# Optimization experiments

Hardware: AMD Instinct MI355X
Metric: run time of the kernel (lower is better)

The kernel has to match this reference:

```python
import jax, jax.numpy as jnp
import numpy as np

B, A, E = 16384, 8, 512


def setup_inputs() -> dict:
    key = jax.random.key(0)
    ks = jax.random.split(key, 6)
    return {
        "image_features": jax.random.normal(ks[0], (B, E), dtype=jnp.float32),
        "edge_attributes": jax.random.normal(ks[1], (B, A, E), dtype=jnp.float32),
        "linear_w": jax.random.normal(ks[2], (E, 2 * E), dtype=jnp.float32) * (1.0 / np.sqrt(2 * E)),
        "linear_b": jax.random.normal(ks[3], (E,), dtype=jnp.float32) * 0.01,
        "fwd_proj": jax.random.normal(ks[4], (A, E, E), dtype=jnp.float32) * (1.0 / np.sqrt(E)),
        "bwd_proj": jax.random.normal(ks[5], (A, E, E), dtype=jnp.float32) * (1.0 / np.sqrt(E)),
        "self_weighted": jnp.ones((1, A, 1), dtype=jnp.float32),
    }


def reference(image_features, edge_attributes, linear_w, linear_b, fwd_proj, bwd_proj, self_weighted):
    # Forward attribute GNN: broadcast src over attribute axis, concat, linear(2E->E)
    src = jnp.broadcast_to(image_features[:, None, :], edge_attributes.shape)  # [B,A,E]
    x = jnp.concatenate([src, edge_attributes], axis=-1)                       # [B,A,2E]
    agg = jnp.einsum('bak,ek->bae', x, linear_w) + linear_b                    # [B,A,E]
    attr_rep = jnp.einsum('bai,aij->baj', agg, fwd_proj)                       # [B,A,E]

    # Backward attribute GNN: per-type projection, ReLU, learned weighted sum over A
    proj = jnp.einsum('bai,aij->baj', attr_rep, bwd_proj)                      # [B,A,E]
    individuals = jnp.sum(jax.nn.relu(proj) * self_weighted, axis=1)           # [B,E]
    return attr_rep, individuals
```

## Files before the change

### kernel.cpp

```cpp
#include <hip/hip_runtime.h>
#include <cstdint>
#include <cstddef>

#define NB 16384
#define NA 8
#define NE 512
#define NK 1024
#define NN 4096

typedef __bf16 bf16x8 __attribute__((ext_vector_type(8)));
typedef float  f32x4  __attribute__((ext_vector_type(4)));
typedef uint16_t u16x8 __attribute__((ext_vector_type(8)));

__device__ __forceinline__ uint16_t cvt_bf16(float f) {
    uint32_t u = __builtin_bit_cast(uint32_t, f);
    u += 0x7fffu + ((u >> 16) & 1u);
    return (uint16_t)(u >> 16);
}

__device__ __forceinline__ int swz(int row) { return (row ^ (row >> 2)) & 3; }

__device__ __forceinline__ int cf_pos(int row, int c) {
    return ((row >> 1) << 3) + ((((row & 1) << 2) + c) ^ ((row >> 1) & 7));
}

__device__ __forceinline__ void gl_lds16(const void* g, void* l) {
    __builtin_amdgcn_global_load_lds(
        (__attribute__((address_space(1))) void*)(void*)g,
        (__attribute__((address_space(3))) void*)l, 16, 0, 0);
}

__device__ __forceinline__ void tcvt_tile(const float* __restrict__ src,
                                          uint16_t* __restrict__ dst,
                                          int R, int C, int c0, int r0, int t) {
    __shared__ float tile[32][33];
    int tx = t & 31, ty = t >> 5;
#pragma unroll
    for (int yy = 0; yy < 4; ++yy) {
        int r = ty + yy * 8;
        tile[r][tx] = src[(size_t)(r0 + r) * C + c0 + tx];
    }
    __syncthreads();
#pragma unroll
    for (int yy = 0; yy < 4; ++yy) {
        int c = ty + yy * 8;
        dst[(size_t)(c0 + c) * R + r0 + tx] = cvt_bf16(tile[tx][c]);
    }
}

__global__ __launch_bounds__(256) void k_pre(const float* __restrict__ lw,
                                             const float* __restrict__ fwd,
                                             const float* __restrict__ bwd,
                                             const float* __restrict__ img,
                                             const float* __restrict__ lb,
                                             uint16_t* __restrict__ lwT,
                                             uint16_t* __restrict__ fwdT,
                                             uint16_t* __restrict__ bwdT,
                                             uint16_t* __restrict__ imgb,
                                             float* __restrict__ bvec) {
    int b = blockIdx.x, t = threadIdx.x;
    if (b < 512) {
        int bx = b & 31, by = b >> 5;
        tcvt_tile(lw, lwT, NE, NK, bx * 32, by * 32, t);
    } else if (b < 2560) {
        int i = b - 512;
        int mat = i >> 8, bx = i & 15, by = (i >> 4) & 15;
        tcvt_tile(fwd + (size_t)mat * NE * NE, fwdT + (size_t)mat * NE * NE,
                  NE, NE, bx * 32, by * 32, t);
    } else if (b < 4608) {
        int i = b - 2560;
        int mat = i >> 8, bx = i & 15, by = (i >> 4) & 15;
        tcvt_tile(bwd + (size_t)mat * NE * NE, bwdT + (size_t)mat * NE * NE,
                  NE, NE, bx * 32, by * 32, t);
    } else if (b < 12800) {
        int i = (b - 4608) * 256 + t;
        float4 v = ((const float4*)img)[i];
        ushort4 o;
        o.x = cvt_bf16(v.x); o.y = cvt_bf16(v.y); o.z = cvt_bf16(v.z); o.w = cvt_bf16(v.w);
        ((ushort4*)imgb)[i] = o;
    } else {
        int i = b - 12800;
        int a = i >> 4, i0 = (i & 15) * 32;
        float s0 = 0.f, s1 = 0.f;
#pragma unroll 4
        for (int k = 0; k < 32; ++k) {
            float w = lb[i0 + k];
            const float* f = fwd + ((size_t)a * NE + i0 + k) * NE;
            s0 = fmaf(w, f[t], s0);
            s1 = fmaf(w, f[t + 256], s1);
        }
        atomicAdd(&bvec[a * NE + t], s0);
        atomicAdd(&bvec[a * NE + t + 256], s1);
    }
}

__global__ __launch_bounds__(256) void k_prep(const uint16_t* __restrict__ lwT,
                                              const uint16_t* __restrict__ fwdT,
                                              uint16_t* __restrict__ TMT) {
    __shared__ alignas(16) uint16_t lA[128 * 32];
    __shared__ alignas(16) uint16_t lB[128 * 32];
    int bz = blockIdx.x;
    int nt = bz & 31, mt = bz >> 5;
    int m0 = mt * 128, n0 = nt * 128;
    int t = threadIdx.x, lane = t & 63;
    int w = t >> 6, wm = w >> 1, wn = w & 1;
    int lr = lane & 15, lc = lane >> 4;
    int sl = swz(lr);
    f32x4 acc[4][4] = {};
    for (int k0 = 0; k0 < NE; k0 += 32) {
        __syncthreads();
#pragma unroll
        for (int p = 0; p < 2; ++p) {
            int idx = p * 256 + t;
            int row = idx >> 2, c16 = (idx & 3) ^ swz(row);
            gl_lds16(lwT + (size_t)(m0 + row) * NE + k0 + c16 * 8, lA + idx * 8);
            gl_lds16(fwdT + (size_t)(n0 + row) * NE + k0 + c16 * 8, lB + idx * 8);
        }
        __syncthreads();
        bf16x8 af[4], bfr[4];
#pragma unroll
        for (int i = 0; i < 4; ++i)
            af[i] = *(const bf16x8*)&lA[(wm * 64 + i * 16 + lr) * 32 + ((lc ^ sl) << 3)];
#pragma unroll
        for (int j = 0; j < 4; ++j)
            bfr[j] = *(const bf16x8*)&lB[(wn * 64 + j * 16 + lr) * 32 + ((lc ^ sl) << 3)];
#pragma unroll
        for (int i = 0; i < 4; ++i)
#pragma unroll
            for (int j = 0; j < 4; ++j)
                acc[i][j] = __builtin_amdgcn_mfma_f32_16x16x32_bf16(af[i], bfr[j], acc[i][j], 0, 0, 0);
    }
#pragma unroll
    for (int i = 0; i < 4; ++i) {
        int mb = m0 + wm * 64 + i * 16 + lc * 4;
#pragma unroll
        for (int j = 0; j < 4; ++j) {
            int n = n0 + wn * 64 + j * 16 + lr;
            ushort4 v;
            v.x = cvt_bf16(acc[i][j][0]);
            v.y = cvt_bf16(acc[i][j][1]);
            v.z = cvt_bf16(acc[i][j][2]);
            v.w = cvt_bf16(acc[i][j][3]);
            *(ushort4*)&TMT[(size_t)n * NK + mb] = v;
        }
    }
}

template<bool WB>
__global__ __launch_bounds__(512) void k_mm4(const uint16_t* __restrict__ imgb,
                                             const float* __restrict__ edge,
                                             const uint16_t* __restrict__ TMT,
                                             const float* __restrict__ bvec,
                                             float* __restrict__ attr,
                                             uint16_t* __restrict__ attrb) {
    __shared__ alignas(16) uint16_t lA[2][128 * 32];
    __shared__ alignas(16) uint16_t lB[2][256 * 32];
    int o = blockIdx.x;
    int a = o & 7, idx = o >> 3;
    int jt = idx & 1, mt = idx >> 1;
    int m0 = mt * 128, jb = jt * 256;
    int t = threadIdx.x, lane = t & 63;
    int w = t >> 6, wm = w >> 2, wn = w & 3;
    int lr = lane & 15, lc = lane >> 4;
    int rpA = t >> 3, qA = (t & 7) ^ (rpA & 7);
    int srA = (rpA << 1) | (qA >> 2), scA = (qA & 3) << 3;
    int srB[2], scB[2];
#pragma unroll
    for (int p = 0; p < 2; ++p) {
        int u = t + p * 512;
        int rp = u >> 3, q = (u & 7) ^ (rp & 7);
        srB[p] = (rp << 1) | (q >> 2);
        scB[p] = (q & 3) << 3;
    }
    int er = t >> 2, ec = t & 3;
    int epos = cf_pos(er, ec) * 8;
    int aoff[4], boff[4];
#pragma unroll
    for (int i = 0; i < 4; ++i) {
        aoff[i] = cf_pos(wm * 64 + i * 16 + lr, lc) * 8;
        boff[i] = cf_pos(wn * 64 + i * 16 + lr, lc) * 8;
    }
    auto stage_img = [&](int buf, int s) {
        gl_lds16(imgb + (size_t)(m0 + srA) * NE + s * 32 + scA, &lA[buf][t * 8]);
    };
    auto stage_tmt = [&](int buf, int s) {
#pragma unroll
        for (int p = 0; p < 2; ++p)
            gl_lds16(TMT + (size_t)(a * NE + jb + srB[p]) * NK + s * 32 + scB[p],
                     &lB[buf][(t + p * 512) * 8]);
    };
    f32x4 acc[4][4] = {};
    stage_img(0, 0);
    stage_tmt(0, 0);
    for (int s = 0; s < 32; ++s) {
        int cur = s & 1, nb = cur ^ 1;
        __syncthreads();
        float4 e0, e1;
        bool eN = (s < 31) && (s + 1 >= 16);
        if (s < 31) {
            if (s + 1 < 16) {
                stage_img(nb, s + 1);
            } else {
                int kk = (s + 1 - 16) * 32;
                const float* sp = edge + ((size_t)(m0 + er) * NA + a) * NE + kk + ec * 8;
                e0 = ((const float4*)sp)[0];
                e1 = ((const float4*)sp)[1];
            }
            stage_tmt(nb, s + 1);
        }
        bf16x8 af[4], bfr[4];
#pragma unroll
        for (int i = 0; i < 4; ++i) af[i] = *(const bf16x8*)&lA[cur][aoff[i]];
#pragma unroll
        for (int j = 0; j < 4; ++j) bfr[j] = *(const bf16x8*)&lB[cur][boff[j]];
#pragma unroll
        for (int i = 0; i < 4; ++i)
#pragma unroll
            for (int j = 0; j < 4; ++j)
                acc[i][j] = __builtin_amdgcn_mfma_f32_16x16x32_bf16(af[i], bfr[j], acc[i][j], 0, 0, 0);
        if (eN) {
            u16x8 ov = {cvt_bf16(e0.x), cvt_bf16(e0.y), cvt_bf16(e0.z), cvt_bf16(e0.w),
                        cvt_bf16(e1.x), cvt_bf16(e1.y), cvt_bf16(e1.z), cvt_bf16(e1.w)};
            *(u16x8*)&lA[nb][epos] = ov;
        }
    }
#pragma unroll
    for (int j = 0; j < 4; ++j) {
        float bv = bvec[a * NE + jb + wn * 64 + j * 16 + lr];
#pragma unroll
        for (int i = 0; i < 4; ++i)
#pragma unroll
            for (int r = 0; r < 4; ++r)
                acc[i][j][r] += bv;
    }
#pragma unroll
    for (int i = 0; i < 4; ++i) {
#pragma unroll
        for (int r = 0; r < 4; ++r) {
            int bm = m0 + wm * 64 + i * 16 + lc * 4 + r;
            float* orow = attr + ((size_t)bm * NA + a) * NE + jb;
#pragma unroll
            for (int j = 0; j < 4; ++j)
                __builtin_nontemporal_store(acc[i][j][r], &orow[wn * 64 + j * 16 + lr]);
            if (WB) {
                uint16_t* brw = attrb + ((size_t)bm * NA + a) * NE + jb;
#pragma unroll
                for (int j = 0; j < 4; ++j)
                    brw[wn * 64 + j * 16 + lr] = cvt_bf16(acc[i][j][r]);
            }
        }
    }
}

template<bool AB>
__global__ __launch_bounds__(256) void k_ind4(const float* __restrict__ attrf,
                                              const uint16_t* __restrict__ attrb,
                                              const uint16_t* __restrict__ bwdT,
                                              const float* __restrict__ sw,
                                              float* __restrict__ ind) {
    __shared__ alignas(16) uint16_t lA[2][128 * 32];
    __shared__ alignas(16) uint16_t lB[2][128 * 32];
    int o = blockIdx.x;
    int xcd = o & 7, mt = o >> 3;
    int jt = xcd >> 1, ah = xcd & 1;
    int m0 = mt * 128, jb = jt * 128, a0 = ah * 4;
    int t = threadIdx.x, lane = t & 63;
    int w = t >> 6, wm = w >> 1, wn = w & 1;
    int lr = lane & 15, lc = lane >> 4;
    int srow[2], sc8[2];
#pragma unroll
    for (int p = 0; p < 2; ++p) {
        int u = p * 256 + t;
        int rp = u >> 3, q = (u & 7) ^ (rp & 7);
        srow[p] = (rp << 1) | (q >> 2);
        sc8[p] = (q & 3) << 3;
    }
    int erow[2], ec[2], epos[2];
#pragma unroll
    for (int p = 0; p < 2; ++p) {
        int u = p * 256 + t;
        erow[p] = u >> 2; ec[p] = u & 3;
        epos[p] = cf_pos(erow[p], ec[p]) * 8;
    }
    int aoff[4], boff[4];
#pragma unroll
    for (int i = 0; i < 4; ++i) {
        aoff[i] = cf_pos(wm * 64 + i * 16 + lr, lc) * 8;
        boff[i] = cf_pos(wn * 64 + i * 16 + lr, lc) * 8;
    }
    auto stage = [&](int buf, int s) {
        int aa = a0 + (s >> 4), kk = (s & 15) * 32;
        if (AB) {
#pragma unroll
            for (int p = 0; p < 2; ++p)
                gl_lds16(attrb + ((size_t)(m0 + srow[p]) * NA + aa) * NE + kk + sc8[p],
                         &lA[buf][(p * 256 + t) * 8]);
        } else {
#pragma unroll
            for (int p = 0; p < 2; ++p) {
                const float* sp = attrf + ((size_t)(m0 + erow[p]) * NA + aa) * NE + kk + ec[p] * 8;
                float4 v0 = ((const float4*)sp)[0];
                float4 v1 = ((const float4*)sp)[1];
                u16x8 ov = {cvt_bf16(v0.x), cvt_bf16(v0.y), cvt_bf16(v0.z), cvt_bf16(v0.w),
                            cvt_bf16(v1.x), cvt_bf16(v1.y), cvt_bf16(v1.z), cvt_bf16(v1.w)};
                *(u16x8*)&lA[buf][epos[p]] = ov;
            }
        }
#pragma unroll
        for (int p = 0; p < 2; ++p)
            gl_lds16(bwdT + (size_t)(aa * NE + jb + srow[p]) * NE + kk + sc8[p],
                     &lB[buf][(p * 256 + t) * 8]);
    };
    f32x4 res[4][4] = {};
    f32x4 acc[4][4] = {};
    stage(0, 0);
    for (int s = 0; s < 64; ++s) {
        int cur = s & 1;
        __syncthreads();
        if (s < 63) stage(cur ^ 1, s + 1);
        bf16x8 af[4], bfr[4];
#pragma unroll
        for (int i = 0; i < 4; ++i) af[i] = *(const bf16x8*)&lA[cur][aoff[i]];
#pragma unroll
        for (int j = 0; j < 4; ++j) bfr[j] = *(const bf16x8*)&lB[cur][boff[j]];
#pragma unroll
        for (int i = 0; i < 4; ++i)
#pragma unroll
            for (int j = 0; j < 4; ++j)
                acc[i][j] = __builtin_amdgcn_mfma_f32_16x16x32_bf16(af[i], bfr[j], acc[i][j], 0, 0, 0);
        if ((s & 15) == 15) {
            float wa = sw[a0 + (s >> 4)];
#pragma unroll
            for (int i = 0; i < 4; ++i)
#pragma unroll
                for (int j = 0; j < 4; ++j) {
#pragma unroll
                    for (int r = 0; r < 4; ++r)
                        res[i][j][r] += wa * fmaxf(acc[i][j][r], 0.f);
                    acc[i][j] = (f32x4){0.f, 0.f, 0.f, 0.f};
                }
        }
    }
#pragma unroll
    for (int i = 0; i < 4; ++i) {
#pragma unroll
        for (int r = 0; r < 4; ++r) {
            int bm = m0 + wm * 64 + i * 16 + lc * 4 + r;
            float* orow = ind + (size_t)bm * NE + jb;
#pragma unroll
            for (int j = 0; j < 4; ++j)
                atomicAdd(&orow[wn * 64 + j * 16 + lr], res[i][j][r]);
        }
    }
}

extern "C" void kernel_launch(void* const* d_in, const int* in_sizes, int n_in,
                              void* d_out, int out_size, void* d_ws, size_t ws_size,
                              hipStream_t stream) {
    (void)in_sizes; (void)n_in; (void)out_size;
    const float* img  = (const float*)d_in[0];
    const float* edge = (const float*)d_in[1];
    const float* lw   = (const float*)d_in[2];
    const float* lb   = (const float*)d_in[3];
    const float* fwd  = (const float*)d_in[4];
    const float* bwd  = (const float*)d_in[5];
    const float* sw   = (const float*)d_in[6];
    float* attr = (float*)d_out;
    float* ind  = attr + (size_t)NB * NA * NE;

    char* ws = (char*)d_ws;
    size_t off = 0;
    auto alloc = [&](size_t bytes) { void* p = ws + off; off += bytes; return p; };
    uint16_t* lwT  = (uint16_t*)alloc((size_t)NK * NE * 2);
    uint16_t* fwdT = (uint16_t*)alloc((size_t)NA * NE * NE * 2);
    uint16_t* bwdT = (uint16_t*)alloc((size_t)NA * NE * NE * 2);
    uint16_t* TMT  = (uint16_t*)alloc((size_t)NN * NK * 2);
    uint16_t* imgb = (uint16_t*)alloc((size_t)NB * NE * 2);
    float*    bvec = (float*)alloc((size_t)NN * 4);

    const size_t BIGB = (size_t)NB * NA * NE * 2;
    bool has_attrb = ws_size >= off + BIGB;
    uint16_t* attrb = has_attrb ? (uint16_t*)alloc(BIGB) : (uint16_t*)0;

    hipMemsetAsync(bvec, 0, (size_t)NN * 4, stream);
    hipMemsetAsync(ind, 0, (size_t)NB * NE * 4, stream);

    k_pre<<<12928, 256, 0, stream>>>(lw, fwd, bwd, img, lb, lwT, fwdT, bwdT, imgb, bvec);
    k_prep<<<(NK / 128) * (NN / 128), 256, 0, stream>>>(lwT, fwdT, TMT);

    int mm_grid = 8 * 2 * (NB / 128);
    int ind_grid = (NB / 128) * (NE / 128) * 2;

    if (has_attrb) {
        k_mm4<true><<<mm_grid, 512, 0, stream>>>(imgb, edge, TMT, bvec, attr, attrb);
        k_ind4<true><<<ind_grid, 256, 0, stream>>>(attr, attrb, bwdT, sw, ind);
    } else {
        k_mm4<false><<<mm_grid, 512, 0, stream>>>(imgb, edge, TMT, bvec, attr, attrb);
        k_ind4<false><<<ind_grid, 256, 0, stream>>>(attr, attrb, bwdT, sw, ind);
    }
}
```

Before: 440.6 us.

## Pre-convert edge attributes to bf16 and use triple-buffered async-LDS GEMM

Adds a pre-pass in k_pre that converts the large edge_attributes tensor to bf16 in workspace. A new k_mm10 kernel then streams both A and B operands with direct global-to-LDS loads in 64-wide K chunks, triple-buffered with swizzled LDS. The aim is to drop the fp32 register-staged conversion from the main GEMM and overlap loads with MFMA. The cost is an extra full pass over edge (read fp32, write bf16) and extra workspace, and the path only runs when the workspace is large enough.

```diff
diff --git a/kernel.cpp b/kernel.cpp
--- a/kernel.cpp
+++ b/kernel.cpp
@@ -53,11 +53,13 @@
                                              const float* __restrict__ bwd,
                                              const float* __restrict__ img,
                                              const float* __restrict__ lb,
+                                             const float* __restrict__ edge,
                                              uint16_t* __restrict__ lwT,
                                              uint16_t* __restrict__ fwdT,
                                              uint16_t* __restrict__ bwdT,
                                              uint16_t* __restrict__ imgb,
-                                             float* __restrict__ bvec) {
+                                             float* __restrict__ bvec,
+                                             uint16_t* __restrict__ edgeb) {
     int b = blockIdx.x, t = threadIdx.x;
     if (b < 512) {
         int bx = b & 31, by = b >> 5;
@@ -78,7 +80,7 @@
         ushort4 o;
         o.x = cvt_bf16(v.x); o.y = cvt_bf16(v.y); o.z = cvt_bf16(v.z); o.w = cvt_bf16(v.w);
         ((ushort4*)imgb)[i] = o;
-    } else {
+    } else if (b < 12928) {
         int i = b - 12800;
         int a = i >> 4, i0 = (i & 15) * 32;
         float s0 = 0.f, s1 = 0.f;
@@ -91,6 +93,14 @@
         }
         atomicAdd(&bvec[a * NE + t], s0);
         atomicAdd(&bvec[a * NE + t + 256], s1);
+    } else {
+        size_t i8 = (size_t)(b - 12928) * 256 + t;
+        const float* sp = edge + i8 * 8;
+        float4 v0 = ((const float4*)sp)[0];
+        float4 v1 = ((const float4*)sp)[1];
+        u16x8 o = {cvt_bf16(v0.x), cvt_bf16(v0.y), cvt_bf16(v0.z), cvt_bf16(v0.w),
+                   cvt_bf16(v1.x), cvt_bf16(v1.y), cvt_bf16(v1.z), cvt_bf16(v1.w)};
+        *(u16x8*)(edgeb + i8 * 8) = o;
     }
 }
 
@@ -142,6 +152,128 @@
             v.z = cvt_bf16(acc[i][j][2]);
             v.w = cvt_bf16(acc[i][j][3]);
             *(ushort4*)&TMT[(size_t)n * NK + mb] = v;
+        }
+    }
+}
+
+template<bool WB>
+__global__ __launch_bounds__(512) void k_mm10(const uint16_t* __restrict__ imgb,
+                                              const uint16_t* __restrict__ edgeb,
+                                              const uint16_t* __restrict__ TMT,
+                                              const float* __restrict__ bvec,
+                                              float* __restrict__ attr,
+                                              uint16_t* __restrict__ attrb) {
+    __shared__ alignas(16) uint16_t lA[3][128 * 64];
+    __shared__ alignas(16) uint16_t lB[3][256 * 64];
+    int o = blockIdx.x;
+    int a = o & 7, idx = o >> 3;
+    int jt = idx & 1, mt = idx >> 1;
+    int m0 = mt * 128, jb = jt * 256;
+    int t = threadIdx.x, lane = t & 63;
+    int w = t >> 6, wm = w >> 2, wn = w & 3;
+    int lr = lane & 15, lc = lane >> 4;
+    int srA[2], scA[2];
+#pragma unroll
+    for (int p = 0; p < 2; ++p) {
+        int u = t + p * 512;
+        srA[p] = u >> 3;
+        scA[p] = ((u & 7) ^ (srA[p] & 7)) << 3;
+    }
+    int srB[4], scB[4];
+#pragma unroll
+    for (int p = 0; p < 4; ++p) {
+        int u = t + p * 512;
+        srB[p] = u >> 3;
+        scB[p] = ((u & 7) ^ (srB[p] & 7)) << 3;
+    }
+    int arow[4], brow[4];
+#pragma unroll
+    for (int i = 0; i < 4; ++i) {
+        arow[i] = wm * 64 + i * 16 + lr;
+        brow[i] = wn * 64 + i * 16 + lr;
+    }
+    f32x4 acc[4][4] = {};
+
+    auto stage = [&](int buf, int k) {
+        if (k < 8) {
+#pragma unroll
+            for (int p = 0; p < 2; ++p)
+                gl_lds16(imgb + (size_t)(m0 + srA[p]) * NE + k * 64 + scA[p],
+                         &lA[buf][(t + p * 512) * 8]);
+        } else {
+#pragma unroll
+            for (int p = 0; p < 2; ++p)
+                gl_lds16(edgeb + ((size_t)(m0 + srA[p]) * NA + a) * NE + (k - 8) * 64 + scA[p],
+                         &lA[buf][(t + p * 512) * 8]);
+        }
+#pragma unroll
+        for (int p = 0; p < 4; ++p)
+            gl_lds16(TMT + (size_t)(a * NE + jb + srB[p]) * NK + k * 64 + scB[p],
+                     &lB[buf][(t + p * 512) * 8]);
+    };
+    auto compute = [&](int cur) {
+        bf16x8 af[4][2], bfr[4][2];
+#pragma unroll
+        for (int i = 0; i < 4; ++i)
+#pragma unroll
+            for (int h = 0; h < 2; ++h)
+                af[i][h] = *(const bf16x8*)&lA[cur][(arow[i] << 6) + ((((h << 2) + lc) ^ (arow[i] & 7)) << 3)];
+#pragma unroll
+        for (int j = 0; j < 4; ++j)
+#pragma unroll
+            for (int h = 0; h < 2; ++h)
+                bfr[j][h] = *(const bf16x8*)&lB[cur][(brow[j] << 6) + ((((h << 2) + lc) ^ (brow[j] & 7)) << 3)];
+        asm volatile("s_waitcnt lgkmcnt(0)" ::: "memory");
+        __builtin_amdgcn_sched_barrier(0);
+#pragma unroll
+        for (int h = 0; h < 2; ++h)
+#pragma unroll
+            for (int i = 0; i < 4; ++i)
+#pragma unroll
+                for (int j = 0; j < 4; ++j)
+                    acc[i][j] = __builtin_amdgcn_mfma_f32_16x16x32_bf16(af[i][h], bfr[j][h], acc[i][j], 0, 0, 0);
+    };
+
+    stage(0, 0);
+    stage(1, 1);
+    stage(2, 2);
+    for (int k = 0; k < 14; ++k) {
+        int cur = k % 3;
+        asm volatile("s_waitcnt vmcnt(12)\n\ts_barrier" ::: "memory");
+        compute(cur);
+        asm volatile("s_barrier" ::: "memory");
+        if (k < 13) stage(cur, k + 3);
+    }
+    asm volatile("s_waitcnt vmcnt(6)\n\ts_barrier" ::: "memory");
+    compute(2);
+    asm volatile("s_barrier" ::: "memory");
+    asm volatile("s_waitcnt vmcnt(0)\n\ts_barrier" ::: "memory");
+    compute(0);
+
+#pragma unroll
+    for (int j = 0; j < 4; ++j) {
+        float bv = bvec[a * NE + jb + wn * 64 + j * 16 + lr];
+#pragma unroll
+        for (int i = 0; i < 4; ++i)
+#pragma unroll
+            for (int r = 0; r < 4; ++r)
+                acc[i][j][r] += bv;
+    }
+#pragma unroll
+    for (int i = 0; i < 4; ++i) {
+#pragma unroll
+        for (int r = 0; r < 4; ++r) {
+            int bm = m0 + wm * 64 + i * 16 + lc * 4 + r;
+            float* orow = attr + ((size_t)bm * NA + a) * NE + jb;
+#pragma unroll
+            for (int j = 0; j < 4; ++j)
+                __builtin_nontemporal_store(acc[i][j][r], &orow[wn * 64 + j * 16 + lr]);
+            if (WB) {
+                uint16_t* brw = attrb + ((size_t)bm * NA + a) * NE + jb;
+#pragma unroll
+                for (int j = 0; j < 4; ++j)
+                    brw[wn * 64 + j * 16 + lr] = cvt_bf16(acc[i][j][r]);
+            }
         }
     }
 }
@@ -381,21 +513,33 @@
     const size_t BIGB = (size_t)NB * NA * NE * 2;
     bool has_attrb = ws_size >= off + BIGB;
     uint16_t* attrb = has_attrb ? (uint16_t*)alloc(BIGB) : (uint16_t*)0;
+    bool has_edgeb = ws_size >= off + BIGB;
+    uint16_t* edgeb = has_edgeb ? (uint16_t*)alloc(BIGB) : (uint16_t*)0;
 
     hipMemsetAsync(bvec, 0, (size_t)NN * 4, stream);
     hipMemsetAsync(ind, 0, (size_t)NB * NE * 4, stream);
 
-    k_pre<<<12928, 256, 0, stream>>>(lw, fwd, bwd, img, lb, lwT, fwdT, bwdT, imgb, bvec);
+    int pre_grid = has_edgeb ? 45696 : 12928;
+    k_pre<<<pre_grid, 256, 0, stream>>>(lw, fwd, bwd, img, lb, edge,
+                                        lwT, fwdT, bwdT, imgb, bvec, edgeb);
     k_prep<<<(NK / 128) * (NN / 128), 256, 0, stream>>>(lwT, fwdT, TMT);
 
     int mm_grid = 8 * 2 * (NB / 128);
     int ind_grid = (NB / 128) * (NE / 128) * 2;
 
-    if (has_attrb) {
-        k_mm4<true><<<mm_grid, 512, 0, stream>>>(imgb, edge, TMT, bvec, attr, attrb);
+    if (has_edgeb) {
+        if (has_attrb)
+            k_mm10<true><<<mm_grid, 512, 0, stream>>>(imgb, edgeb, TMT, bvec, attr, attrb);
+        else
+            k_mm10<false><<<mm_grid, 512, 0, stream>>>(imgb, edgeb, TMT, bvec, attr, attrb);
+    } else {
+        if (has_attrb)
+            k_mm4<true><<<mm_grid, 512, 0, stream>>>(imgb, edge, TMT, bvec, attr, attrb);
+        else
+            k_mm4<false><<<mm_grid, 512, 0, stream>>>(imgb, edge, TMT, bvec, attr, attrb);
+    }
+    if (has_attrb)
         k_ind4<true><<<ind_grid, 256, 0, stream>>>(attr, attrb, bwdT, sw, ind);
-    } else {
-        k_mm4<false><<<mm_grid, 512, 0, stream>>>(imgb, edge, TMT, bvec, attr, attrb);
+    else
         k_ind4<false><<<ind_grid, 256, 0, stream>>>(attr, attrb, bwdT, sw, ind);
-    }
-}
+}
```

Result: slower. 450.0 us (+2.1%).
